# Performance work log

Hardware: AMD Instinct MI355X
Metric: run time of the kernel (lower is better)

The kernel has to match this reference:

```python
import jax, jax.numpy as jnp
import numpy as np
from jax import lax

B, T_IN, T_OUT = 32, 400, 500
N_MEL, ENC, RNN, PRE, ATT, LOC_F, LOC_K = 80, 512, 1024, 256, 128, 32, 31


def setup_inputs() -> dict:
    key = jax.random.key(0)
    ks = jax.random.split(key, 16)
    s = 0.02
    p = lambda i, sh: (jax.random.normal(ks[i], sh) * s).astype(jnp.float32)
    memory = jax.random.normal(ks[0], (B, T_IN, ENC), dtype=jnp.float32)
    decoder_inputs = jax.random.normal(ks[1], (B, N_MEL, T_OUT), dtype=jnp.float32)
    memory_lengths = jax.random.randint(ks[2], (B,), T_IN // 2, T_IN + 1).at[0].set(T_IN).astype(jnp.int32)
    return {
        'memory': memory,
        'decoder_inputs': decoder_inputs,
        'memory_lengths': memory_lengths,
        'prenet_w1': p(3, (PRE, N_MEL)),
        'prenet_w2': p(4, (PRE, PRE)),
        'att_wih': p(5, (4 * RNN, PRE + ENC)),
        'att_whh': p(6, (4 * RNN, RNN)),
        'att_bih': jnp.zeros((4 * RNN,), jnp.float32),
        'att_bhh': jnp.zeros((4 * RNN,), jnp.float32),
        'query_w': p(7, (ATT, RNN)),
        'memory_w': p(8, (ATT, ENC)),
        'v_w': p(9, (1, ATT)),
        'loc_conv_w': p(10, (LOC_F, 2, LOC_K)),
        'loc_lin_w': p(11, (ATT, LOC_F)),
        'dec_wih': p(12, (4 * RNN, RNN + ENC)),
        'dec_whh': p(13, (4 * RNN, RNN)),
        'dec_bih': jnp.zeros((4 * RNN,), jnp.float32),
        'dec_bhh': jnp.zeros((4 * RNN,), jnp.float32),
        'proj_w': p(14, (N_MEL, RNN + ENC)),
        'proj_b': jnp.zeros((N_MEL,), jnp.float32),
        'gate_w': p(15, (1, RNN + ENC)),
        'gate_b': jnp.zeros((1,), jnp.float32),
    }


def _lstm(x, h, c, wih, whh, bih, bhh):
    g = x @ wih.T + h @ whh.T + bih + bhh
    i, f, gg, o = jnp.split(g, 4, axis=-1)
    c2 = jax.nn.sigmoid(f) * c + jax.nn.sigmoid(i) * jnp.tanh(gg)
    return jax.nn.sigmoid(o) * jnp.tanh(c2), c2


def _forward(memory, decoder_inputs, memory_lengths, prenet_w1, prenet_w2,
             att_wih, att_whh, att_bih, att_bhh, query_w, memory_w, v_w,
             loc_conv_w, loc_lin_w, dec_wih, dec_whh, dec_bih, dec_bhh,
             proj_w, proj_b, gate_w, gate_b):
    # deterministic dropout masks (prenet p=0.5 always on; rnn dropout p=0.1, training mode)
    k1, k2, k3, k4 = jax.random.split(jax.random.key(42), 4)
    # teacher-forced inputs: [B,80,T_out] -> [T_out,B,80], prepend all-zero go frame
    dec_in = jnp.transpose(decoder_inputs, (2, 0, 1))
    dec_in = jnp.concatenate([jnp.zeros((1, B, N_MEL), decoder_inputs.dtype), dec_in], axis=0)
    x = dec_in
    for w, k in ((prenet_w1, k1), (prenet_w2, k2)):
        x = jax.nn.relu(x @ w.T)
        x = jnp.where(jax.random.bernoulli(k, 0.5, x.shape), x * 2.0, 0.0)
    prenet_out = x[:T_OUT]  # one decode step per target frame
    att_drop = jnp.where(jax.random.bernoulli(k3, 0.9, (T_OUT, B, RNN)), 1.0 / 0.9, 0.0).astype(jnp.float32)
    dec_drop = jnp.where(jax.random.bernoulli(k4, 0.9, (T_OUT, B, RNN)), 1.0 / 0.9, 0.0).astype(jnp.float32)
    processed_memory = memory @ memory_w.T  # [B,T_in,ATT]
    valid = jnp.arange(T_IN)[None, :] < memory_lengths[:, None]  # [B,T_in]
    pad = (LOC_K - 1) // 2

    def step(carry, xs):
        ah, ac, dh, dc, aw, awc, ctx = carry
        din, am, dm = xs
        ah, ac = _lstm(jnp.concatenate([din, ctx], -1), ah, ac, att_wih, att_whh, att_bih, att_bhh)
        ah = ah * am
        cat = jnp.stack([aw, awc], axis=1)  # [B,2,T_in]
        loc = lax.conv_general_dilated(cat, loc_conv_w, (1,), [(pad, pad)], dimension_numbers=('NCH', 'OIH', 'NCH'))
        loc = jnp.einsum('bft,af->bta', loc, loc_lin_w)  # [B,T_in,ATT]
        pq = (ah @ query_w.T)[:, None, :]  # [B,1,ATT]
        e = jnp.tanh(pq + loc + processed_memory) @ v_w[0]  # [B,T_in]
        e = jnp.where(valid, e, -jnp.inf)
        aw2 = jax.nn.softmax(e, axis=1)
        ctx2 = jnp.einsum('bt,btd->bd', aw2, memory)
        awc2 = awc + aw2
        dh, dc = _lstm(jnp.concatenate([ah, ctx2], -1), dh, dc, dec_wih, dec_whh, dec_bih, dec_bhh)
        dh = dh * dm
        hc = jnp.concatenate([dh, ctx2], -1)
        mel = hc @ proj_w.T + proj_b
        gate = (hc @ gate_w.T + gate_b)[:, 0]
        return (ah, ac, dh, dc, aw2, awc2, ctx2), (mel, gate, aw2)

    z = lambda *sh: jnp.zeros(sh, jnp.float32)
    carry0 = (z(B, RNN), z(B, RNN), z(B, RNN), z(B, RNN), z(B, T_IN), z(B, T_IN), z(B, ENC))
    _, (mels, gates, aligns) = lax.scan(step, carry0, (prenet_out, att_drop, dec_drop))
    mel_outputs = jnp.transpose(mels, (1, 2, 0))      # [B, n_mel, T_out]
    gate_outputs = gates.T                             # [B, T_out]
    alignments = jnp.transpose(aligns, (1, 0, 2))      # [B, T_out, T_in]
    return mel_outputs, gate_outputs, alignments


def reference(memory, decoder_inputs, memory_lengths, prenet_w1, prenet_w2,
              att_wih, att_whh, att_bih, att_bhh, query_w, memory_w, v_w,
              loc_conv_w, loc_lin_w, dec_wih, dec_whh, dec_bih, dec_bhh,
              proj_w, proj_b, gate_w, gate_b):
    return _forward(memory, decoder_inputs, memory_lengths, prenet_w1, prenet_w2,
                    att_wih, att_whh, att_bih, att_bhh, query_w, memory_w, v_w,
                    loc_conv_w, loc_lin_w, dec_wih, dec_whh, dec_bih, dec_bhh,
                    proj_w, proj_b, gate_w, gate_b)
```

## Files before the change

kernel.cpp:

```cpp
#include <hip/hip_runtime.h>
#include <cstdint>

typedef unsigned short ushortT;
typedef __attribute__((ext_vector_type(8))) short s8v;
typedef __attribute__((ext_vector_type(4))) float f4v;

#define TIN 400
#define TOUT 500

__host__ __device__ __forceinline__ uint32_t rotl32(uint32_t v, int r){ return (v<<r)|(v>>(32-r)); }
__host__ __device__ inline void tf2x32(uint32_t k0, uint32_t k1, uint32_t x0, uint32_t x1,
                                       uint32_t* o0, uint32_t* o1){
  uint32_t ks2 = k0 ^ k1 ^ 0x1BD11BDAu;
  x0 += k0; x1 += k1;
  x0+=x1; x1=rotl32(x1,13); x1^=x0;  x0+=x1; x1=rotl32(x1,15); x1^=x0;
  x0+=x1; x1=rotl32(x1,26); x1^=x0;  x0+=x1; x1=rotl32(x1, 6); x1^=x0;
  x0+=k1; x1+=ks2+1u;
  x0+=x1; x1=rotl32(x1,17); x1^=x0;  x0+=x1; x1=rotl32(x1,29); x1^=x0;
  x0+=x1; x1=rotl32(x1,16); x1^=x0;  x0+=x1; x1=rotl32(x1,24); x1^=x0;
  x0+=ks2; x1+=k0+2u;
  x0+=x1; x1=rotl32(x1,13); x1^=x0;  x0+=x1; x1=rotl32(x1,15); x1^=x0;
  x0+=x1; x1=rotl32(x1,26); x1^=x0;  x0+=x1; x1=rotl32(x1, 6); x1^=x0;
  x0+=k0; x1+=k1+3u;
  x0+=x1; x1=rotl32(x1,17); x1^=x0;  x0+=x1; x1=rotl32(x1,29); x1^=x0;
  x0+=x1; x1=rotl32(x1,16); x1^=x0;  x0+=x1; x1=rotl32(x1,24); x1^=x0;
  x0+=k1; x1+=ks2+4u;
  x0+=x1; x1=rotl32(x1,13); x1^=x0;  x0+=x1; x1=rotl32(x1,15); x1^=x0;
  x0+=x1; x1=rotl32(x1,26); x1^=x0;  x0+=x1; x1=rotl32(x1, 6); x1^=x0;
  x0+=ks2; x1+=k0+5u;
  *o0 = x0; *o1 = x1;
}
__device__ __forceinline__ float part_unif(uint32_t ka, uint32_t kb, uint32_t idx){
  uint32_t o0,o1; tf2x32(ka,kb,0u,idx,&o0,&o1);
  uint32_t bits = o0 ^ o1;
  return __uint_as_float(0x3f800000u | (bits>>9)) - 1.0f;
}

__device__ __forceinline__ float bf2f(ushortT u){ return __uint_as_float(((uint32_t)u)<<16); }
__device__ __forceinline__ ushortT f2bf(float f){
  uint32_t x = __float_as_uint(f);
  return (ushortT)((x + 0x7fffu + ((x>>16)&1u)) >> 16);
}
__device__ __forceinline__ float sigm(float x){ return 1.0f/(1.0f+__expf(-x)); }
__device__ __forceinline__ f4v mfma16(s8v a, s8v b, f4v c){
  return __builtin_amdgcn_mfma_f32_16x16x32_bf16(a,b,c,0,0,0);
}
__device__ __forceinline__ s8v pack8(const float* p){
  s8v r;
  #pragma unroll
  for (int j=0;j<8;++j) r[j]=(short)f2bf(p[j]);
  return r;
}
__device__ __forceinline__ uint32_t ld32_sc1(const void* ptr){
  return __hip_atomic_load((uint32_t*)ptr, __ATOMIC_RELAXED, __HIP_MEMORY_SCOPE_AGENT);
}
__device__ __forceinline__ float ldf_sc1(const float* ptr){
  return __uint_as_float(ld32_sc1(ptr));
}
__device__ __forceinline__ s8v ld8_sc1(const ushortT* ptr){
  union { s8v v; unsigned long long q[2]; } u;
  u.q[0] = __hip_atomic_load((unsigned long long*)ptr,     __ATOMIC_RELAXED, __HIP_MEMORY_SCOPE_AGENT);
  u.q[1] = __hip_atomic_load((unsigned long long*)ptr + 1, __ATOMIC_RELAXED, __HIP_MEMORY_SCOPE_AGENT);
  return u.v;
}

__global__ __launch_bounds__(256) void k_setup(
  const float* __restrict__ memory, const float* __restrict__ qw,
  const float* __restrict__ pjw,  const float* __restrict__ gw,
  ushortT* __restrict__ Mbf, ushortT* __restrict__ Wq, ushortT* __restrict__ Wpg,
  ushortT* __restrict__ AH0, ushortT* __restrict__ AH1,
  ushortT* __restrict__ DH0, ushortT* __restrict__ DH1,
  ushortT* __restrict__ CT0, ushortT* __restrict__ CT1,
  float* __restrict__ aw, float* __restrict__ awc,
  uint32_t* __restrict__ bars)
{
  int stride = gridDim.x*blockDim.x;
  int g0 = blockIdx.x*blockDim.x + threadIdx.x;
  for (int i=g0; i<32*400*512; i+=stride) Mbf[i]=f2bf(memory[i]);
  for (int i=g0; i<128*1024;  i+=stride) Wq[i]=f2bf(qw[i]);
  for (int i=g0; i<96*1536; i+=stride){
    int r=i/1536, k=i-r*1536;
    ushortT v=0;
    if (r<80) v=f2bf(pjw[r*1536+k]);
    else if (r==80) v=f2bf(gw[k]);
    Wpg[i]=v;
  }
  for (int i=g0; i<32*1024; i+=stride){ AH0[i]=0; AH1[i]=0; DH0[i]=0; DH1[i]=0; }
  for (int i=g0; i<32*512;  i+=stride){ CT0[i]=0; CT1[i]=0; }
  for (int i=g0; i<32*400;  i+=stride){ aw[i]=0.f; awc[i]=0.f; }
  if (g0 < 512) bars[g0]=0u;
}

__global__ __launch_bounds__(256) void k_prenet(
  const float* __restrict__ dec_inp, const float* __restrict__ w1, const float* __restrict__ w2,
  ushortT* __restrict__ preo,
  uint32_t k1a, uint32_t k1b, uint32_t k2a, uint32_t k2b)
{
  __shared__ ushortT Xs[64*96];
  __shared__ ushortT H1s[64*256];
  int tid=threadIdx.x, lane=tid&63, wv=tid>>6, quad=lane>>4, nl=lane&15;
  int r0 = blockIdx.x*64;
  for (int i=tid; i<64*96; i+=256){
    int rr=i/96, k=i-rr*96; int row=r0+rr; int s=row>>5, b=row&31;
    float v=0.f;
    if (k<80 && s>0) v = dec_inp[((size_t)b*80+k)*500 + (s-1)];
    Xs[i]=f2bf(v);
  }
  __syncthreads();
  f4v acc[4][4];
  #pragma unroll
  for (int mtl=0;mtl<4;++mtl)
    #pragma unroll
    for (int nt=0;nt<4;++nt) acc[mtl][nt]=(f4v){0,0,0,0};
  for (int kb=0;kb<3;++kb){
    int c0 = kb*32 + quad*8;
    s8v a[4];
    #pragma unroll
    for (int mtl=0;mtl<4;++mtl) a[mtl]=*(const s8v*)(Xs + (mtl*16+nl)*96 + c0);
    #pragma unroll
    for (int nt=0;nt<4;++nt){
      int rown = wv*64+nt*16+nl;
      s8v bb;
      if (c0 < 80) bb = pack8(w1 + (size_t)rown*80 + c0);
      else { s8v z={0,0,0,0,0,0,0,0}; bb=z; }
      #pragma unroll
      for (int mtl=0;mtl<4;++mtl) acc[mtl][nt]=mfma16(a[mtl],bb,acc[mtl][nt]);
    }
  }
  #pragma unroll
  for (int mtl=0;mtl<4;++mtl)
    #pragma unroll
    for (int nt=0;nt<4;++nt)
      #pragma unroll
      for (int r=0;r<4;++r){
        int mloc = mtl*16+quad*4+r;
        int col  = wv*64+nt*16+nl;
        float v = acc[mtl][nt][r]; v = v>0.f? v:0.f;
        uint32_t fidx = (uint32_t)(r0+mloc)*256u + (uint32_t)col;
        v = (part_unif(k1a,k1b,fidx) < 0.5f) ? v*2.0f : 0.0f;
        H1s[mloc*256+col]=f2bf(v);
      }
  __syncthreads();
  #pragma unroll
  for (int mtl=0;mtl<4;++mtl)
    #pragma unroll
    for (int nt=0;nt<4;++nt) acc[mtl][nt]=(f4v){0,0,0,0};
  for (int kb=0;kb<8;++kb){
    int c0 = kb*32 + quad*8;
    s8v a[4];
    #pragma unroll
    for (int mtl=0;mtl<4;++mtl) a[mtl]=*(const s8v*)(H1s + (mtl*16+nl)*256 + c0);
    #pragma unroll
    for (int nt=0;nt<4;++nt){
      int rown = wv*64+nt*16+nl;
      s8v bb = pack8(w2 + (size_t)rown*256 + c0);
      #pragma unroll
      for (int mtl=0;mtl<4;++mtl) acc[mtl][nt]=mfma16(a[mtl],bb,acc[mtl][nt]);
    }
  }
  #pragma unroll
  for (int mtl=0;mtl<4;++mtl)
    #pragma unroll
    for (int nt=0;nt<4;++nt)
      #pragma unroll
      for (int r=0;r<4;++r){
        int mloc = mtl*16+quad*4+r;
        int col  = wv*64+nt*16+nl;
        float v = acc[mtl][nt][r]; v = v>0.f? v:0.f;
        uint32_t fidx = (uint32_t)(r0+mloc)*256u + (uint32_t)col;
        v = (part_unif(k2a,k2b,fidx) < 0.5f) ? v*2.0f : 0.0f;
        preo[(size_t)(r0+mloc)*256+col]=f2bf(v);
      }
}

__global__ __launch_bounds__(256) void k_pm(
  const float* __restrict__ memory, const float* __restrict__ mw, float* __restrict__ pm)
{
  int row = blockIdx.x*2 + (threadIdx.x>>7);
  int col = threadIdx.x & 127;
  const float* mr = memory + (size_t)row*512;
  const float* wr = mw + (size_t)col*512;
  float acc=0.f;
  for (int k=0;k<512;k+=4){
    float4 a=*(const float4*)(mr+k), b=*(const float4*)(wr+k);
    acc += a.x*b.x + a.y*b.y + a.z*b.z + a.w*b.w;
  }
  pm[(size_t)row*128+col]=acc;
}

struct PArgs {
  const float* awih; const float* awhh; const float* abih; const float* abhh;
  const float* dwih; const float* dwhh; const float* dbih; const float* dbhh;
  const float* lcw;  const float* llw;  const float* vw;
  const float* pjb;  const float* gb;
  const float* pm;   const int* mlen;
  const ushortT* preo; const ushortT* Wq; const ushortT* Wpg; const ushortT* Mbf;
  ushortT* AH0; ushortT* AH1; ushortT* DH0; ushortT* DH1; ushortT* CT0; ushortT* CT1;
  float* aw; float* awc; float* ebuf;
  float* out_mel; float* out_gate; float* out_align;
  uint32_t* bars;
  uint32_t katt_a, katt_b, kdec_a, kdec_b;
};

__device__ __forceinline__ void gridbar(uint32_t* bars, uint32_t* myg){
  __syncthreads();
  if (threadIdx.x == 0){
    uint32_t g = *myg + 1u; *myg = g;
    __builtin_amdgcn_fence(__ATOMIC_RELEASE, "agent");
    uint32_t* gc  = bars + 32u*(blockIdx.x & 7u);
    uint32_t* mc  = bars + 256u;
    uint32_t* gen = bars + 288u;
    uint32_t prev = __hip_atomic_fetch_add(gc,1u,__ATOMIC_RELAXED,__HIP_MEMORY_SCOPE_AGENT);
    bool setter=false;
    if (prev == g*32u - 1u){
      uint32_t p2 = __hip_atomic_fetch_add(mc,1u,__ATOMIC_RELAXED,__HIP_MEMORY_SCOPE_AGENT);
      if (p2 == g*8u - 1u){
        __hip_atomic_store(gen, g, __ATOMIC_RELAXED, __HIP_MEMORY_SCOPE_AGENT);
        setter=true;
      }
    }
    if (!setter){
      while (__hip_atomic_load(gen, __ATOMIC_RELAXED, __HIP_MEMORY_SCOPE_AGENT) < g){
        __builtin_amdgcn_s_sleep(2);
      }
    }
  }
  __syncthreads();
}

__global__ __launch_bounds__(256,1) void k_persist(PArgs p){
  __shared__ ushortT Wa[16*1800];
  __shared__ ushortT Wd[16*2568];
  __shared__ float gbufA[2][16][33];
  __shared__ float gbufD[2][16][33];
  __shared__ float acst[4][32];
  __shared__ float dcst[4][32];
  __shared__ float biasA[16];
  __shared__ float biasD[16];
  __shared__ float sc[3400];

  const int tid = threadIdx.x;
  const int bid = blockIdx.x;
  const int lane = tid & 63;
  const int wv = tid >> 6;
  const int quad = lane >> 4;
  const int nl = lane & 15;
  const int mt = wv & 1;
  const int kh = wv >> 1;

  for (int rl=0; rl<16; ++rl){
    const int r = (rl>>2)*1024 + bid*4 + (rl&3);
    for (int c=tid; c<1792; c+=256){
      float v = (c<768) ? p.awih[(size_t)r*768+c] : p.awhh[(size_t)r*1024+(c-768)];
      Wa[rl*1800+c] = f2bf(v);
    }
    for (int c=tid; c<2560; c+=256){
      float v = (c<1536) ? p.dwih[(size_t)r*1536+c] : p.dwhh[(size_t)r*1024+(c-1536)];
      Wd[rl*2568+c] = f2bf(v);
    }
  }
  if (tid < 16){
    int g=tid>>2, u=bid*4+(tid&3);
    biasA[tid]=p.abih[g*1024+u]+p.abhh[g*1024+u];
    biasD[tid]=p.dbih[g*1024+u]+p.dbhh[g*1024+u];
  }
  if (tid < 128){ acst[tid>>5][tid&31]=0.f; dcst[tid>>5][tid&31]=0.f; }
  __syncthreads();

  uint32_t myg = 0;

  for (int t=0; t<=TOUT; ++t){
    const ushortT* AHp = (t&1)? p.AH0 : p.AH1;
    ushortT*       AHn = (t&1)? p.AH1 : p.AH0;
    const ushortT* DHi = (t&1)? p.DH1 : p.DH0;
    ushortT*       DHo = (t&1)? p.DH0 : p.DH1;
    const ushortT* CTXp= (t&1)? p.CT1 : p.CT0;
    ushortT*       CTXn= (t&1)? p.CT0 : p.CT1;

    const int arow = mt*16 + nl;
    if (t < TOUT){
      const ushortT* Xp = p.preo + ((size_t)t*32 + arow)*256 + quad*8;
      const ushortT* Xc = CTXp + arow*512 + quad*8;
      const ushortT* Xa = AHp + arow*1024 + quad*8;
      const ushortT* wr = Wa + nl*1800 + quad*8;
      f4v acc = {0.f,0.f,0.f,0.f};
      if (kh==0){
        #pragma unroll
        for (int kb=0;kb<8;++kb)  acc = mfma16(*(const s8v*)(Xp+kb*32), *(const s8v*)(wr+kb*32), acc);
        #pragma unroll
        for (int kb=0;kb<16;++kb) acc = mfma16(ld8_sc1(Xc+kb*32), *(const s8v*)(wr+256+kb*32), acc);
        #pragma unroll
        for (int kb=0;kb<4;++kb)  acc = mfma16(ld8_sc1(Xa+kb*32), *(const s8v*)(wr+768+kb*32), acc);
      } else {
        #pragma unroll
        for (int kb=0;kb<28;++kb) acc = mfma16(ld8_sc1(Xa+128+kb*32), *(const s8v*)(wr+896+kb*32), acc);
      }
      #pragma unroll
      for (int r4=0;r4<4;++r4) gbufA[kh][nl][mt*16+quad*4+r4]=acc[r4];
    }
    if (t >= 1){
      const ushortT* Xa = AHp + arow*1024 + quad*8;
      const ushortT* Xc = CTXp + arow*512 + quad*8;
      const ushortT* Xd = DHi + arow*1024 + quad*8;
      const ushortT* wr = Wd + nl*2568 + quad*8;
      f4v acc = {0.f,0.f,0.f,0.f};
      if (kh==0){
        #pragma unroll
        for (int kb=0;kb<32;++kb) acc = mfma16(ld8_sc1(Xa+kb*32), *(const s8v*)(wr+kb*32), acc);
        #pragma unroll
        for (int kb=0;kb<8;++kb)  acc = mfma16(ld8_sc1(Xc+kb*32), *(const s8v*)(wr+1024+kb*32), acc);
      } else {
        #pragma unroll
        for (int kb=0;kb<8;++kb)  acc = mfma16(ld8_sc1(Xc+256+kb*32), *(const s8v*)(wr+1280+kb*32), acc);
        #pragma unroll
        for (int kb=0;kb<32;++kb) acc = mfma16(ld8_sc1(Xd+kb*32), *(const s8v*)(wr+1536+kb*32), acc);
      }
      #pragma unroll
      for (int r4=0;r4<4;++r4) gbufD[kh][nl][mt*16+quad*4+r4]=acc[r4];
    }
    __syncthreads();
    if (t < TOUT && tid < 128){
      const int uu=tid>>5, b=tid&31, u=bid*4+uu;
      float gi=gbufA[0][uu][b]   +gbufA[1][uu][b]   +biasA[uu];
      float gf=gbufA[0][4+uu][b] +gbufA[1][4+uu][b] +biasA[4+uu];
      float gg=gbufA[0][8+uu][b] +gbufA[1][8+uu][b] +biasA[8+uu];
      float go=gbufA[0][12+uu][b]+gbufA[1][12+uu][b]+biasA[12+uu];
      float cp=acst[uu][b];
      float c2=sigm(gf)*cp+sigm(gi)*tanhf(gg);
      float h =sigm(go)*tanhf(c2);
      uint32_t fidx=((uint32_t)(t*32+b))*1024u+(uint32_t)u;
      h=(part_unif(p.katt_a,p.katt_b,fidx)<0.9f)? h*(1.0f/0.9f):0.f;
      acst[uu][b]=c2;
      AHn[b*1024+u]=f2bf(h);
    }
    if (t >= 1 && tid >= 128){
      const int uu=(tid>>5)&3, b=tid&31, u=bid*4+uu;
      float gi=gbufD[0][uu][b]   +gbufD[1][uu][b]   +biasD[uu];
      float gf=gbufD[0][4+uu][b] +gbufD[1][4+uu][b] +biasD[4+uu];
      float gg=gbufD[0][8+uu][b] +gbufD[1][8+uu][b] +biasD[8+uu];
      float go=gbufD[0][12+uu][b]+gbufD[1][12+uu][b]+biasD[12+uu];
      float cp=dcst[uu][b];
      float c2=sigm(gf)*cp+sigm(gi)*tanhf(gg);
      float h =sigm(go)*tanhf(c2);
      uint32_t fidx=((uint32_t)((t-1)*32+b))*1024u+(uint32_t)u;
      h=(part_unif(p.kdec_a,p.kdec_b,fidx)<0.9f)? h*(1.0f/0.9f):0.f;
      dcst[uu][b]=c2;
      DHo[b*1024+u]=f2bf(h);
    }
    gridbar(p.bars,&myg);

    if (bid < 128){
      if (t < TOUT){
        const int b = bid>>2, ch = bid&3, t0 = ch*100;
        float* xA = (float*)gbufA;
        float* xD = (float*)gbufD;
        ushortT* sAH = (ushortT*)xA;
        {
          const uint32_t* ahsrc = (const uint32_t*)(AHn + b*1024);
          for (int i=tid;i<512;i+=256) ((uint32_t*)sAH)[i] = ld32_sc1(ahsrc + i);
        }
        for (int i=tid;i<130;i+=256){
          int tt=t0-15+i; float a_=0.f,c_=0.f;
          if (tt>=0 && tt<TIN){ a_=ldf_sc1(p.aw + b*TIN+tt); c_=ldf_sc1(p.awc + b*TIN+tt); }
          xD[i]=a_; xD[130+i]=c_;
        }
        __syncthreads();
        {
          const int a=tid&127, half=tid>>7;
          const ushortT* qr = p.Wq + a*1024 + half*512;
          const ushortT* hr = sAH + half*512;
          float acc=0.f;
          for (int k=0;k<512;k+=8){
            s8v q=*(const s8v*)(qr+k);
            s8v h=*(const s8v*)(hr+k);
            #pragma unroll
            for (int j=0;j<8;++j) acc += bf2f((ushortT)q[j])*bf2f((ushortT)h[j]);
          }
          xA[512+tid]=acc;
        }
        for (int it=tid; it<3200; it+=256){
          const int tl=it>>5, f=it&31;
          const float* c0p=p.lcw + (f*2)*31;
          const float* c1p=c0p + 31;
          float s=0.f;
          #pragma unroll
          for (int j=0;j<31;++j) s += xD[tl+j]*c0p[j] + xD[130+tl+j]*c1p[j];
          sc[tl*32+f]=s;
        }
        __syncthreads();
        if (tid<128) xA[768+tid]=xA[512+tid]+xA[512+128+tid];
        __syncthreads();
        {
          const int a_=tid&127, g=tid>>7, wid=tid>>6;
          float lw_r[32];
          #pragma unroll
          for (int j=0;j<32;++j) lw_r[j]=p.llw[a_*32+j];
          const float vr = p.vw[a_];
          const float pqa = xA[768+a_];
          for (int tl=g; tl<100; tl+=2){
            const float* lt = sc + tl*32;
            float l2=0.f;
            #pragma unroll
            for (int f=0;f<32;++f) l2 += lt[f]*lw_r[f];
            float x = pqa + l2 + p.pm[((size_t)b*TIN + (t0+tl))*128 + a_];
            x = fminf(fmaxf(x,-30.f),30.f);
            float ex = __expf(2.f*x);
            float cv = vr*((ex-1.f)*__builtin_amdgcn_rcpf(ex+1.f));
            #pragma unroll
            for (int o=32;o>0;o>>=1) cv += __shfl_xor(cv,o);
            if ((tid&63)==0) xD[260 + tl*2 + (wid&1)]=cv;
          }
        }
        __syncthreads();
        if (tid<100){
          const int tg=t0+tid;
          float e = xD[260+tid*2] + xD[260+tid*2+1];
          float pv = (tg < p.mlen[b]) ? __expf(e) : 0.f;
          p.ebuf[b*TIN+tg]=pv;
        }
      }
    } else if (bid < 134){
      if (t >= 1){
        const int td=t-1, rb=(bid-128)*16;
        const int mrow = nl + mt*16;
        const ushortT* br  = p.Wpg + (size_t)(rb+nl)*1536 + quad*8;
        const ushortT* dhp = DHo + (size_t)mrow*1024 + quad*8;
        const ushortT* cxp = CTXp + (size_t)mrow*512 + quad*8;
        f4v acc={0.f,0.f,0.f,0.f};
        for (int kb=0;kb<24;++kb){
          const int kk=kh*768+kb*32;
          s8v aa = (kk<1024)? ld8_sc1(dhp+kk) : ld8_sc1(cxp+(kk-1024));
          acc = mfma16(aa, *(const s8v*)(br+kk), acc);
        }
        #pragma unroll
        for (int r4=0;r4<4;++r4) sc[kh*512 + (mt*16+quad*4+r4)*16 + nl]=acc[r4];
        __syncthreads();
        for (int idx=tid; idx<512; idx+=256){
          const int m=idx>>4, n=idx&15, r=rb+n;
          float v=sc[m*16+n]+sc[512+m*16+n];
          if (r<80) p.out_mel[(size_t)(m*80+r)*500+td]=v+p.pjb[r];
          else if (r==80) p.out_gate[(size_t)m*500+td]=v+p.gb[0];
        }
      }
    }
    gridbar(p.bars,&myg);

    if (t < TOUT){
      const int b = bid>>3, s = bid&7;
      float* pv  = (float*)gbufA;
      float* red = pv + 408;
      for (int i=tid;i<TIN;i+=256) pv[i]=ldf_sc1(p.ebuf + b*TIN + i);
      __syncthreads();
      float ls=0.f;
      for (int i=tid;i<TIN;i+=256) ls+=pv[i];
      #pragma unroll
      for (int o=32;o>0;o>>=1) ls+=__shfl_xor(ls,o);
      if ((tid&63)==0) red[tid>>6]=ls;
      __syncthreads();
      const float S=red[0]+red[1]+red[2]+red[3];
      const float rS=(S>0.f)?1.0f/S:0.f;
      const int dl = tid&63, q = tid>>6;
      const int d = s*64 + dl;
      const ushortT* mb = p.Mbf + ((size_t)b*TIN + q*100)*512 + d;
      const float* pq_ = pv + q*100;
      float cc=0.f;
      #pragma unroll 4
      for (int tt=0;tt<100;++tt) cc += pq_[tt]*bf2f(mb[(size_t)tt*512]);
      sc[q*64+dl]=cc;
      __syncthreads();
      if (q==0){
        float v = sc[dl]+sc[64+dl]+sc[128+dl]+sc[192+dl];
        CTXn[b*512+d]=f2bf(v*rS);
      }
      if (s==0){
        for (int i=tid;i<TIN;i+=256){
          float a2 = pv[i]*rS;
          p.aw[b*TIN+i]=a2;
          p.awc[b*TIN+i]+=a2;
          p.out_align[((size_t)b*500+t)*400+i]=a2;
        }
      }
    }
    gridbar(p.bars,&myg);
  }
}

extern "C" void kernel_launch(void* const* d_in, const int* in_sizes, int n_in,
                              void* d_out, int out_size, void* d_ws, size_t ws_size,
                              hipStream_t stream) {
  (void)in_sizes; (void)n_in; (void)out_size; (void)ws_size;
  const float* memory  = (const float*)d_in[0];
  const float* dec_inp = (const float*)d_in[1];
  const int*   mlen    = (const int*)d_in[2];
  const float* pw1     = (const float*)d_in[3];
  const float* pw2     = (const float*)d_in[4];
  const float* awih    = (const float*)d_in[5];
  const float* awhh    = (const float*)d_in[6];
  const float* abih    = (const float*)d_in[7];
  const float* abhh    = (const float*)d_in[8];
  const float* qw      = (const float*)d_in[9];
  const float* mw      = (const float*)d_in[10];
  const float* vw      = (const float*)d_in[11];
  const float* lcw     = (const float*)d_in[12];
  const float* llw     = (const float*)d_in[13];
  const float* dwih    = (const float*)d_in[14];
  const float* dwhh    = (const float*)d_in[15];
  const float* dbih    = (const float*)d_in[16];
  const float* dbhh    = (const float*)d_in[17];
  const float* pjw     = (const float*)d_in[18];
  const float* pjb     = (const float*)d_in[19];
  const float* gw      = (const float*)d_in[20];
  const float* gb      = (const float*)d_in[21];

  char* w = (char*)d_ws;
  size_t off=0;
  auto alloc = [&](size_t n)->char*{ char* p=w+off; off=(off+n+255)&~(size_t)255; return p; };
  ushortT* Mbf = (ushortT*)alloc(32UL*400*512*2);
  ushortT* Wq  = (ushortT*)alloc(128UL*1024*2);
  ushortT* Wpg = (ushortT*)alloc(96UL*1536*2);
  ushortT* preo= (ushortT*)alloc(16000UL*256*2);
  float*   pm  = (float*)alloc(12800UL*128*4);
  ushortT* AH0 = (ushortT*)alloc(32UL*1024*2);
  ushortT* AH1 = (ushortT*)alloc(32UL*1024*2);
  ushortT* DH0 = (ushortT*)alloc(32UL*1024*2);
  ushortT* DH1 = (ushortT*)alloc(32UL*1024*2);
  ushortT* CT0 = (ushortT*)alloc(32UL*512*2);
  ushortT* CT1 = (ushortT*)alloc(32UL*512*2);
  float*   aw  = (float*)alloc(12800UL*4);
  float*   awc = (float*)alloc(12800UL*4);
  float*   ebuf= (float*)alloc(12800UL*4);
  uint32_t* bars=(uint32_t*)alloc(2048);

  uint32_t K[4][2];
  for (uint32_t i=0;i<4;++i) tf2x32(0u,42u,0u,i,&K[i][0],&K[i][1]);

  float* out_mel   = (float*)d_out;
  float* out_gate  = out_mel + 1280000;
  float* out_align = out_mel + 1296000;

  k_setup<<<1024,256,0,stream>>>(memory,qw,pjw,gw,Mbf,Wq,Wpg,AH0,AH1,DH0,DH1,CT0,CT1,aw,awc,bars);
  k_prenet<<<250,256,0,stream>>>(dec_inp, pw1, pw2, preo, K[0][0],K[0][1], K[1][0],K[1][1]);
  k_pm<<<6400,256,0,stream>>>(memory, mw, pm);

  PArgs pa;
  pa.awih=awih; pa.awhh=awhh; pa.abih=abih; pa.abhh=abhh;
  pa.dwih=dwih; pa.dwhh=dwhh; pa.dbih=dbih; pa.dbhh=dbhh;
  pa.lcw=lcw; pa.llw=llw; pa.vw=vw; pa.pjb=pjb; pa.gb=gb;
  pa.pm=pm; pa.mlen=mlen;
  pa.preo=preo; pa.Wq=Wq; pa.Wpg=Wpg; pa.Mbf=Mbf;
  pa.AH0=AH0; pa.AH1=AH1; pa.DH0=DH0; pa.DH1=DH1; pa.CT0=CT0; pa.CT1=CT1;
  pa.aw=aw; pa.awc=awc; pa.ebuf=ebuf;
  pa.out_mel=out_mel; pa.out_gate=out_gate; pa.out_align=out_align;
  pa.bars=bars;
  pa.katt_a=K[2][0]; pa.katt_b=K[2][1]; pa.kdec_a=K[3][0]; pa.kdec_b=K[3][1];

  void* kargs[] = { &pa };
  (void)hipLaunchCooperativeKernel((const void*)k_persist, dim3(256), dim3(256), kargs, 0u, stream);
}
```

Measured before the change: 42.15 ms.

## Drop grid-barrier release fence, use agent-scope atomic stores, batch loads before MFMAs

Removes the agent-scope release fence in the grid barrier and instead writes all cross-block shared state (hidden states, context, attention energies/weights) with relaxed agent-scope atomic stores. Hidden-state outputs are first staged in LDS and then written as packed 32-bit words. The MFMA loops are restructured to issue four coherent loads before four MFMAs to hide latency. The aim is to cut per-step barrier cost and load stalls across 500 sequential steps, at the risk of memory-ordering correctness without an explicit fence.

Result: slower. 51.01 ms (+21.0%).

```diff
diff --git a/kernel.cpp b/kernel.cpp
--- a/kernel.cpp
+++ b/kernel.cpp
@@ -63,6 +63,12 @@
   u.q[1] = __hip_atomic_load((unsigned long long*)ptr + 1, __ATOMIC_RELAXED, __HIP_MEMORY_SCOPE_AGENT);
   return u.v;
 }
+__device__ __forceinline__ void st32_wt(void* ptr, uint32_t v){
+  __hip_atomic_store((uint32_t*)ptr, v, __ATOMIC_RELAXED, __HIP_MEMORY_SCOPE_AGENT);
+}
+__device__ __forceinline__ void stf_wt(float* ptr, float v){
+  st32_wt(ptr, __float_as_uint(v));
+}
 
 __global__ __launch_bounds__(256) void k_setup(
   const float* __restrict__ memory, const float* __restrict__ qw,
@@ -206,7 +212,6 @@
   __syncthreads();
   if (threadIdx.x == 0){
     uint32_t g = *myg + 1u; *myg = g;
-    __builtin_amdgcn_fence(__ATOMIC_RELEASE, "agent");
     uint32_t* gc  = bars + 32u*(blockIdx.x & 7u);
     uint32_t* mc  = bars + 256u;
     uint32_t* gen = bars + 288u;
@@ -237,7 +242,9 @@
   __shared__ float dcst[4][32];
   __shared__ float biasA[16];
   __shared__ float biasD[16];
-  __shared__ float sc[3400];
+  __shared__ ushortT ahstg[4][32];
+  __shared__ ushortT dhstg[4][32];
+  __shared__ float sc[3200];
 
   const int tid = threadIdx.x;
   const int bid = blockIdx.x;
@@ -288,12 +295,24 @@
         #pragma unroll
         for (int kb=0;kb<8;++kb)  acc = mfma16(*(const s8v*)(Xp+kb*32), *(const s8v*)(wr+kb*32), acc);
         #pragma unroll
-        for (int kb=0;kb<16;++kb) acc = mfma16(ld8_sc1(Xc+kb*32), *(const s8v*)(wr+256+kb*32), acc);
+        for (int kb=0;kb<16;kb+=4){
+          s8v x0=ld8_sc1(Xc+kb*32), x1=ld8_sc1(Xc+(kb+1)*32), x2=ld8_sc1(Xc+(kb+2)*32), x3=ld8_sc1(Xc+(kb+3)*32);
+          acc = mfma16(x0, *(const s8v*)(wr+256+kb*32), acc);
+          acc = mfma16(x1, *(const s8v*)(wr+256+(kb+1)*32), acc);
+          acc = mfma16(x2, *(const s8v*)(wr+256+(kb+2)*32), acc);
+          acc = mfma16(x3, *(const s8v*)(wr+256+(kb+3)*32), acc);
+        }
         #pragma unroll
         for (int kb=0;kb<4;++kb)  acc = mfma16(ld8_sc1(Xa+kb*32), *(const s8v*)(wr+768+kb*32), acc);
       } else {
         #pragma unroll
-        for (int kb=0;kb<28;++kb) acc = mfma16(ld8_sc1(Xa+128+kb*32), *(const s8v*)(wr+896+kb*32), acc);
+        for (int kb=0;kb<28;kb+=4){
+          s8v x0=ld8_sc1(Xa+128+kb*32), x1=ld8_sc1(Xa+128+(kb+1)*32), x2=ld8_sc1(Xa+128+(kb+2)*32), x3=ld8_sc1(Xa+128+(kb+3)*32);
+          acc = mfma16(x0, *(const s8v*)(wr+896+kb*32), acc);
+          acc = mfma16(x1, *(const s8v*)(wr+896+(kb+1)*32), acc);
+          acc = mfma16(x2, *(const s8v*)(wr+896+(kb+2)*32), acc);
+          acc = mfma16(x3, *(const s8v*)(wr+896+(kb+3)*32), acc);
+        }
       }
       #pragma unroll
       for (int r4=0;r4<4;++r4) gbufA[kh][nl][mt*16+quad*4+r4]=acc[r4];
@@ -306,14 +325,38 @@
       f4v acc = {0.f,0.f,0.f,0.f};
       if (kh==0){
         #pragma unroll
-        for (int kb=0;kb<32;++kb) acc = mfma16(ld8_sc1(Xa+kb*32), *(const s8v*)(wr+kb*32), acc);
-        #pragma unroll
-        for (int kb=0;kb<8;++kb)  acc = mfma16(ld8_sc1(Xc+kb*32), *(const s8v*)(wr+1024+kb*32), acc);
+        for (int kb=0;kb<32;kb+=4){
+          s8v x0=ld8_sc1(Xa+kb*32), x1=ld8_sc1(Xa+(kb+1)*32), x2=ld8_sc1(Xa+(kb+2)*32), x3=ld8_sc1(Xa+(kb+3)*32);
+          acc = mfma16(x0, *(const s8v*)(wr+kb*32), acc);
+          acc = mfma16(x1, *(const s8v*)(wr+(kb+1)*32), acc);
+          acc = mfma16(x2, *(const s8v*)(wr+(kb+2)*32), acc);
+          acc = mfma16(x3, *(const s8v*)(wr+(kb+3)*32), acc);
+        }
+        #pragma unroll
+        for (int kb=0;kb<8;kb+=4){
+          s8v x0=ld8_sc1(Xc+kb*32), x1=ld8_sc1(Xc+(kb+1)*32), x2=ld8_sc1(Xc+(kb+2)*32), x3=ld8_sc1(Xc+(kb+3)*32);
+          acc = mfma16(x0, *(const s8v*)(wr+1024+kb*32), acc);
+          acc = mfma16(x1, *(const s8v*)(wr+1024+(kb+1)*32), acc);
+          acc = mfma16(x2, *(const s8v*)(wr+1024+(kb+2)*32), acc);
+          acc = mfma16(x3, *(const s8v*)(wr+1024+(kb+3)*32), acc);
+        }
       } else {
         #pragma unroll
-        for (int kb=0;kb<8;++kb)  acc = mfma16(ld8_sc1(Xc+256+kb*32), *(const s8v*)(wr+1280+kb*32), acc);
-        #pragma unroll
-        for (int kb=0;kb<32;++kb) acc = mfma16(ld8_sc1(Xd+kb*32), *(const s8v*)(wr+1536+kb*32), acc);
+        for (int kb=0;kb<8;kb+=4){
+          s8v x0=ld8_sc1(Xc+256+kb*32), x1=ld8_sc1(Xc+256+(kb+1)*32), x2=ld8_sc1(Xc+256+(kb+2)*32), x3=ld8_sc1(Xc+256+(kb+3)*32);
+          acc = mfma16(x0, *(const s8v*)(wr+1280+kb*32), acc);
+          acc = mfma16(x1, *(const s8v*)(wr+1280+(kb+1)*32), acc);
+          acc = mfma16(x2, *(const s8v*)(wr+1280+(kb+2)*32), acc);
+          acc = mfma16(x3, *(const s8v*)(wr+1280+(kb+3)*32), acc);
+        }
+        #pragma unroll
+        for (int kb=0;kb<32;kb+=4){
+          s8v x0=ld8_sc1(Xd+kb*32), x1=ld8_sc1(Xd+(kb+1)*32), x2=ld8_sc1(Xd+(kb+2)*32), x3=ld8_sc1(Xd+(kb+3)*32);
+          acc = mfma16(x0, *(const s8v*)(wr+1536+kb*32), acc);
+          acc = mfma16(x1, *(const s8v*)(wr+1536+(kb+1)*32), acc);
+          acc = mfma16(x2, *(const s8v*)(wr+1536+(kb+2)*32), acc);
+          acc = mfma16(x3, *(const s8v*)(wr+1536+(kb+3)*32), acc);
+        }
       }
       #pragma unroll
       for (int r4=0;r4<4;++r4) gbufD[kh][nl][mt*16+quad*4+r4]=acc[r4];
@@ -331,7 +374,7 @@
       uint32_t fidx=((uint32_t)(t*32+b))*1024u+(uint32_t)u;
       h=(part_unif(p.katt_a,p.katt_b,fidx)<0.9f)? h*(1.0f/0.9f):0.f;
       acst[uu][b]=c2;
-      AHn[b*1024+u]=f2bf(h);
+      ahstg[uu][b]=f2bf(h);
     }
     if (t >= 1 && tid >= 128){
       const int uu=(tid>>5)&3, b=tid&31, u=bid*4+uu;
@@ -345,7 +388,18 @@
       uint32_t fidx=((uint32_t)((t-1)*32+b))*1024u+(uint32_t)u;
       h=(part_unif(p.kdec_a,p.kdec_b,fidx)<0.9f)? h*(1.0f/0.9f):0.f;
       dcst[uu][b]=c2;
-      DHo[b*1024+u]=f2bf(h);
+      dhstg[uu][b]=f2bf(h);
+    }
+    __syncthreads();
+    if (t < TOUT && tid < 64){
+      const int b=tid>>1, pp=tid&1;
+      uint32_t wd = (uint32_t)ahstg[2*pp][b] | ((uint32_t)ahstg[2*pp+1][b]<<16);
+      st32_wt((uint32_t*)(AHn + b*1024 + bid*4) + pp, wd);
+    }
+    if (t >= 1 && tid >= 64 && tid < 128){
+      const int j=tid-64, b=j>>1, pp=j&1;
+      uint32_t wd = (uint32_t)dhstg[2*pp][b] | ((uint32_t)dhstg[2*pp+1][b]<<16);
+      st32_wt((uint32_t*)(DHo + b*1024 + bid*4) + pp, wd);
     }
     gridbar(p.bars,&myg);
 
@@ -416,7 +470,7 @@
           const int tg=t0+tid;
           float e = xD[260+tid*2] + xD[260+tid*2+1];
           float pv = (tg < p.mlen[b]) ? __expf(e) : 0.f;
-          p.ebuf[b*TIN+tg]=pv;
+          stf_wt(p.ebuf + b*TIN + tg, pv);
         }
       }
     } else if (bid < 134){
@@ -468,15 +522,19 @@
       for (int tt=0;tt<100;++tt) cc += pq_[tt]*bf2f(mb[(size_t)tt*512]);
       sc[q*64+dl]=cc;
       __syncthreads();
-      if (q==0){
-        float v = sc[dl]+sc[64+dl]+sc[128+dl]+sc[192+dl];
-        CTXn[b*512+d]=f2bf(v*rS);
+      if (tid < 32){
+        const int dl0=tid*2, dl1=dl0+1;
+        float v0 = (sc[dl0]+sc[64+dl0]+sc[128+dl0]+sc[192+dl0])*rS;
+        float v1 = (sc[dl1]+sc[64+dl1]+sc[128+dl1]+sc[192+dl1])*rS;
+        uint32_t wd = (uint32_t)f2bf(v0) | ((uint32_t)f2bf(v1)<<16);
+        st32_wt((uint32_t*)(CTXn + b*512 + s*64) + tid, wd);
       }
       if (s==0){
         for (int i=tid;i<TIN;i+=256){
           float a2 = pv[i]*rS;
-          p.aw[b*TIN+i]=a2;
-          p.awc[b*TIN+i]+=a2;
+          stf_wt(p.aw + b*TIN + i, a2);
+          float oldc = ldf_sc1(p.awc + b*TIN + i);
+          stf_wt(p.awc + b*TIN + i, oldc + a2);
           p.out_align[((size_t)b*500+t)*400+i]=a2;
         }
       }
```
